# Kernel tuning notes

Hardware: AMD Instinct MI355X
Metric: run time of the kernel (lower is better)

The kernel has to match this reference:

```python
import jax, jax.numpy as jnp
import numpy as np

B, N, C = 256, 256, 128   # batch (=N_res rows), seq len, pair channels
H, D = 4, 128             # heads, per-head dim (== output_dim per module code)
O = 128                   # output_dim


def _glorot(key, shape, fan_in, fan_out):
    limit = np.sqrt(6.0 / (fan_in + fan_out))
    return jax.random.uniform(key, shape, jnp.float32, -limit, limit)


def setup_inputs() -> dict:
    key = jax.random.key(0)
    ks = jax.random.split(key, 9)
    q_data = jax.random.normal(ks[0], (B, N, C), jnp.float32)
    m_data = jax.random.normal(ks[1], (B, N, C), jnp.float32)
    bias = jax.random.normal(ks[2], (B, 1, N, N), jnp.float32)
    nonbatched_bias = jax.random.normal(ks[3], (H, N, N), jnp.float32)
    query_w = _glorot(ks[4], (C, H, D), C, H * D)
    key_w = _glorot(ks[5], (C, H, D), C, H * D)
    value_w = _glorot(ks[6], (C, H, D), C, H * D)
    gating_w = jnp.zeros((C, H, D), jnp.float32)
    gating_b = jnp.ones((H, D), jnp.float32)
    output_w = _glorot(ks[7], (H, D, O), H * D, O)
    output_b = jnp.zeros((O,), jnp.float32)
    return {
        'q_data': q_data, 'm_data': m_data, 'bias': bias,
        'nonbatched_bias': nonbatched_bias,
        'query_w': query_w, 'key_w': key_w, 'value_w': value_w,
        'gating_w': gating_w, 'gating_b': gating_b,
        'output_w': output_w, 'output_b': output_b,
    }


def reference(q_data, m_data, bias, nonbatched_bias,
              query_w, key_w, value_w, gating_w, gating_b,
              output_w, output_b):
    key_dim = query_w.shape[-1]  # per-head dim (tied to output_dim in module)
    q = jnp.einsum('bqa,ahc->bqhc', q_data, query_w) * key_dim ** (-0.5)
    k = jnp.einsum('bka,ahc->bkhc', m_data, key_w)
    v = jnp.einsum('bka,ahc->bkhc', m_data, value_w)
    logits = jnp.einsum('bqhc,bkhc->bhqk', q, k) + bias
    logits = logits + nonbatched_bias[None]  # broadcast shared bias over batch
    weights = jax.nn.softmax(logits, axis=-1)
    weighted_avg = jnp.einsum('bhqk,bkhc->bqhc', weights, v)
    gate = jax.nn.sigmoid(jnp.einsum('bqc,chv->bqhv', q_data, gating_w) + gating_b)
    weighted_avg = weighted_avg * gate
    return jnp.einsum('bqhc,hco->bqo', weighted_avg, output_w) + output_b
```

## Files before the change

kernel.cpp:

```cpp
#include <hip/hip_runtime.h>
#include <stdint.h>


typedef unsigned short u16;
typedef u16 u16x8 __attribute__((ext_vector_type(8)));
typedef u16 u16x4 __attribute__((ext_vector_type(4)));
typedef __bf16 bf16x8 __attribute__((ext_vector_type(8)));
typedef float floatx4 __attribute__((ext_vector_type(4)));

union B8 { u16x8 u; bf16x8 b; };

__device__ __forceinline__ float bf2f(u16 u) {
  union { uint32_t i; float f; } v; v.i = ((uint32_t)u) << 16; return v.f;
}
__device__ __forceinline__ u16 f2bf(float f) {
  union { float f; uint32_t i; } v; v.f = f;
  return (u16)((v.i + 0x7fffu + ((v.i >> 16) & 1u)) >> 16);
}
__device__ __forceinline__ bf16x8 ld8(const u16* p) { return *(const bf16x8*)p; }
__device__ __forceinline__ floatx4 mfma16(bf16x8 a, bf16x8 b, floatx4 c) {
  return __builtin_amdgcn_mfma_f32_16x16x32_bf16(a, b, c, 0, 0, 0);
}
__device__ __forceinline__ void cfence() { asm volatile("" ::: "memory"); }

template<bool BF>
__device__ __forceinline__ bf16x8 ldin8(const void* p, long long idx) {
  if constexpr (BF) {
    return *(const bf16x8*)((const u16*)p + idx);
  } else {
    const float* f = (const float*)p + idx;
    floatx4 a = *(const floatx4*)f;
    floatx4 b = *(const floatx4*)(f + 4);
    B8 r;
    #pragma unroll
    for (int i = 0; i < 4; ++i) { r.u[i] = f2bf(a[i]); r.u[i + 4] = f2bf(b[i]); }
    return r.b;
  }
}
template<bool BF>
__device__ __forceinline__ float ldin1(const void* p, long long idx) {
  if constexpr (BF) return bf2f(((const u16*)p)[idx]);
  else              return ((const float*)p)[idx];
}
template<bool BF>
__device__ __forceinline__ floatx4 ldin4(const void* p, long long idx) {
  floatx4 v;
  if constexpr (BF) {
    u16x4 u = *(const u16x4*)((const u16*)p + idx);
    #pragma unroll
    for (int i = 0; i < 4; ++i) v[i] = bf2f(u[i]);
  } else {
    v = *(const floatx4*)((const float*)p + idx);
  }
  return v;
}

template<bool BF>
__device__ __forceinline__ void pre_body(
    const void* qw, const void* kw, const void* vw, const void* gw,
    const void* ow, u16* wt)
{
  const int blk = blockIdx.x, tid = threadIdx.x;
  if (blk < 16) {
    const int mat = blk >> 2, h = blk & 3;
    const void* W = (mat == 0) ? qw : (mat == 1) ? kw : (mat == 2) ? vw : gw;
    u16* dst = wt + blk * 16384;
    for (int idx = tid; idx < 16384; idx += 256) {
      int c = idx >> 7, d = idx & 127;
      dst[d * 128 + c] = f2bf(ldin1<BF>(W, (long long)c * 512 + h * 128 + d));
    }
  } else {
    const int part = blk - 16;
    u16* dst = wt + 16 * 16384;
    for (int idx = tid; idx < 16384; idx += 256) {
      int k = idx >> 7, o = idx & 127;
      int kg = part * 128 + k;
      dst[o * 512 + kg] = f2bf(ldin1<BF>(ow, (long long)kg * 128 + o));
    }
  }
}

__global__ __launch_bounds__(256) void k_pre(
    const void* qw, const void* kw, const void* vw, const void* gw,
    const void* ow, const void* gating_b, u16* wt)
{
  const bool bf = (*(const uint32_t*)gating_b) == 0x3F803F80u;
  if (bf) pre_body<true >(qw, kw, vw, gw, ow, wt);
  else    pre_body<false>(qw, kw, vw, gw, ow, wt);
}

template<bool BF>
__device__ __forceinline__ void fused_body(
    const void* q_data, const void* m_data,
    const void* __restrict__ bias, const void* __restrict__ nbias,
    const void* gating_b, const u16* __restrict__ wt,
    u16* Ob, int b0, int Bc, u16* smem)
{
  const int tid  = threadIdx.x;
  const int lane = tid & 63, w = tid >> 6;
  const int quad = lane >> 4, l15 = lane & 15;
  const int l7   = l15 & 7;

  const int nwg = Bc * 4, id = blockIdx.x;
  const int xcd = id & 7, rest = id >> 3;
  const int qq = nwg >> 3, rm = nwg & 7;
  const int swz = (xcd < rm ? xcd * (qq + 1) : rm * (qq + 1) + (xcd - rm) * qq) + rest;
  const int bl = swz >> 2, h = swz & 3;
  const int bg = b0 + bl;
  const long long bh = (long long)(bl * 4 + h);

  u16* Kl  = smem;
  u16* Vtl = smem + 32768;

  const u16* wtQ = wt + (0 * 4 + h) * 16384;
  const u16* wtK = wt + (1 * 4 + h) * 16384;
  const u16* wtV = wt + (2 * 4 + h) * 16384;
  const u16* wtG = wt + (3 * 4 + h) * 16384;
  const float scale = 0.088388347648318447f;

  const int m0 = w * 16;

  bf16x8 aq[4];
  {
    u16* Qs = (w < 8) ? (Kl + w * 2176) : (Vtl + (w - 8) * 2176);
    floatx4 qa[8];
    #pragma unroll
    for (int ni = 0; ni < 8; ++ni) qa[ni] = (floatx4){0.f, 0.f, 0.f, 0.f};
    #pragma unroll
    for (int ks = 0; ks < 4; ++ks) {
      bf16x8 aA = ldin8<BF>(q_data, ((long long)bg * 256 + m0 + l15) * 128 + ks * 32 + quad * 8);
      #pragma unroll
      for (int ni = 0; ni < 8; ++ni) {
        bf16x8 bw = ld8(wtQ + (ni * 16 + l15) * 128 + ks * 32 + quad * 8);
        qa[ni] = mfma16(aA, bw, qa[ni]);
      }
    }
    #pragma unroll
    for (int ni = 0; ni < 8; ++ni)
      #pragma unroll
      for (int r = 0; r < 4; ++r)
        Qs[(quad * 4 + r) * 136 + ni * 16 + l15] = f2bf(qa[ni][r] * scale);
    cfence();
    #pragma unroll
    for (int ks = 0; ks < 4; ++ks)
      aq[ks] = ld8(Qs + l15 * 136 + ks * 32 + quad * 8);
  }
  __syncthreads();

  {
    bf16x8 aA[4];
    #pragma unroll
    for (int ks = 0; ks < 4; ++ks)
      aA[ks] = ldin8<BF>(m_data, ((long long)bg * 256 + m0 + l15) * 128 + ks * 32 + quad * 8);

    floatx4 ka[8];
    #pragma unroll
    for (int ni = 0; ni < 8; ++ni) ka[ni] = (floatx4){0.f, 0.f, 0.f, 0.f};
    #pragma unroll
    for (int ks = 0; ks < 4; ++ks)
      #pragma unroll
      for (int ni = 0; ni < 8; ++ni) {
        bf16x8 bw = ld8(wtK + (ni * 16 + l15) * 128 + ks * 32 + quad * 8);
        ka[ni] = mfma16(aA[ks], bw, ka[ni]);
      }
    #pragma unroll
    for (int ni = 0; ni < 8; ++ni)
      #pragma unroll
      for (int r = 0; r < 4; ++r) {
        int n = m0 + quad * 4 + r, d = ni * 16 + l15;
        Kl[n * 128 + (d ^ ((n & 7) << 3))] = f2bf(ka[ni][r]);
      }

    floatx4 va[8];
    #pragma unroll
    for (int ni = 0; ni < 8; ++ni) va[ni] = (floatx4){0.f, 0.f, 0.f, 0.f};
    #pragma unroll
    for (int ks = 0; ks < 4; ++ks)
      #pragma unroll
      for (int ni = 0; ni < 8; ++ni) {
        bf16x8 bw = ld8(wtV + (ni * 16 + l15) * 128 + ks * 32 + quad * 8);
        va[ni] = mfma16(aA[ks], bw, va[ni]);
      }
    #pragma unroll
    for (int ni = 0; ni < 8; ++ni) {
      int d = ni * 16 + l15, n4 = m0 + quad * 4;
      u16x4 vv;
      #pragma unroll
      for (int r = 0; r < 4; ++r) vv[r] = f2bf(va[ni][r]);
      *(u16x4*)(Vtl + d * 256 + (n4 ^ ((d & 7) << 3))) = vv;
    }
  }
  __syncthreads();

  floatx4 s[16];
  #pragma unroll
  for (int nt = 0; nt < 16; ++nt) {
    long long gi = ((long long)bg * 256 + m0 + l15) * 256 + nt * 16 + quad * 4;
    long long gn = ((long long)h  * 256 + m0 + l15) * 256 + nt * 16 + quad * 4;
    floatx4 bv = ldin4<BF>(bias, gi);
    floatx4 nv = ldin4<BF>(nbias, gn);
    #pragma unroll
    for (int r = 0; r < 4; ++r) s[nt][r] = bv[r] + nv[r];
  }
  #pragma unroll
  for (int nt = 0; nt < 16; ++nt) {
    #pragma unroll
    for (int ks = 0; ks < 4; ++ks) {
      bf16x8 kf = ld8(Kl + (nt * 16 + l15) * 128 + ((ks * 32 + quad * 8) ^ (l7 << 3)));
      s[nt] = mfma16(kf, aq[ks], s[nt]);
    }
  }

  floatx4 m4 = s[0];
  #pragma unroll
  for (int nt = 1; nt < 16; ++nt)
    #pragma unroll
    for (int r = 0; r < 4; ++r) m4[r] = fmaxf(m4[r], s[nt][r]);
  float mx = fmaxf(fmaxf(m4[0], m4[1]), fmaxf(m4[2], m4[3]));
  mx = fmaxf(mx, __shfl_xor(mx, 16));
  mx = fmaxf(mx, __shfl_xor(mx, 32));

  u16x4 pk[16];
  floatx4 s4 = (floatx4){0.f, 0.f, 0.f, 0.f};
  #pragma unroll
  for (int nt = 0; nt < 16; ++nt) {
    #pragma unroll
    for (int r = 0; r < 4; ++r) {
      float e = __expf(s[nt][r] - mx);
      s4[r] += e;
      pk[nt][r] = f2bf(e);
    }
  }
  float sm = s4[0] + s4[1] + s4[2] + s4[3];
  sm += __shfl_xor(sm, 16);
  sm += __shfl_xor(sm, 32);
  const float inv = 1.f / sm;

  __syncthreads();

  u16* Ps = Kl + w * 2048;
  floatx4 o[8];
  #pragma unroll
  for (int dt = 0; dt < 8; ++dt) o[dt] = (floatx4){0.f, 0.f, 0.f, 0.f};
  #pragma unroll
  for (int kh = 0; kh < 2; ++kh) {
    #pragma unroll
    for (int nt2 = 0; nt2 < 8; ++nt2)
      *(u16x4*)(Ps + l15 * 128 + ((nt2 * 16 + quad * 4) ^ (l7 << 3))) = pk[kh * 8 + nt2];
    cfence();
    bf16x8 ap[4];
    #pragma unroll
    for (int ks = 0; ks < 4; ++ks)
      ap[ks] = ld8(Ps + l15 * 128 + ((ks * 32 + quad * 8) ^ (l7 << 3)));
    #pragma unroll
    for (int dt = 0; dt < 8; ++dt)
      #pragma unroll
      for (int ks = 0; ks < 4; ++ks) {
        bf16x8 bv = ld8(Vtl + (dt * 16 + l15) * 256 +
                        ((kh * 128 + ks * 32 + quad * 8) ^ (l7 << 3)));
        o[dt] = mfma16(ap[ks], bv, o[dt]);
      }
    cfence();
  }

  float invq[4];
  #pragma unroll
  for (int r = 0; r < 4; ++r) invq[r] = __shfl(inv, quad * 4 + r);
  bf16x8 aqd[4];
  #pragma unroll
  for (int ks = 0; ks < 4; ++ks)
    aqd[ks] = ldin8<BF>(q_data, ((long long)bg * 256 + m0 + l15) * 128 + ks * 32 + quad * 8);
  #pragma unroll
  for (int nt = 0; nt < 8; ++nt) {
    floatx4 g = (floatx4){0.f, 0.f, 0.f, 0.f};
    #pragma unroll
    for (int ks = 0; ks < 4; ++ks) {
      bf16x8 bw = ld8(wtG + (nt * 16 + l15) * 128 + ks * 32 + quad * 8);
      g = mfma16(aqd[ks], bw, g);
    }
    #pragma unroll
    for (int r = 0; r < 4; ++r) {
      int row = m0 + quad * 4 + r, d = nt * 16 + l15;
      float gate = 1.f / (1.f + __expf(-(g[r] + ldin1<BF>(gating_b, h * 128 + d))));
      Ob[(bh * 256 + row) * 128 + d] = f2bf(o[nt][r] * invq[r] * gate);
    }
  }
}

__global__ __launch_bounds__(1024) void k_fused(
    const void* q_data, const void* m_data, const void* bias,
    const void* nbias, const void* gating_b, const u16* wt,
    u16* Ob, int b0, int Bc)
{
  __shared__ __align__(16) u16 smem[65536];
  const bool bf = (*(const uint32_t*)gating_b) == 0x3F803F80u;
  if (bf) fused_body<true >(q_data, m_data, bias, nbias, gating_b, wt, Ob, b0, Bc, smem);
  else    fused_body<false>(q_data, m_data, bias, nbias, gating_b, wt, Ob, b0, Bc, smem);
}

template<bool BF>
__device__ __forceinline__ void out_body(
    const u16* wsr, const u16* wtO, const void* output_b,
    void* out, int b0)
{
  const int tid  = threadIdx.x;
  const int lane = tid & 63, w = tid >> 6;
  const int quad = lane >> 4, l15 = lane & 15;
  const int wm = w >> 1, wn = w & 1;
  const int r0l = blockIdx.x * 32;
  const int bl  = r0l >> 8, n0 = r0l & 255;

  floatx4 acc[4];
  #pragma unroll
  for (int ni = 0; ni < 4; ++ni) acc[ni] = (floatx4){0.f, 0.f, 0.f, 0.f};

  #pragma unroll
  for (int kt = 0; kt < 4; ++kt) {
    #pragma unroll
    for (int ks = 0; ks < 4; ++ks) {
      bf16x8 af = ld8(wsr + ((long long)(bl * 4 + kt) * 256 + n0 + wm * 16 + l15) * 128
                          + ks * 32 + quad * 8);
      #pragma unroll
      for (int ni = 0; ni < 4; ++ni) {
        int col = wn * 64 + ni * 16 + l15;
        bf16x8 bw = ld8(wtO + (long long)col * 512 + kt * 128 + ks * 32 + quad * 8);
        acc[ni] = mfma16(af, bw, acc[ni]);
      }
    }
  }

  #pragma unroll
  for (int ni = 0; ni < 4; ++ni) {
    #pragma unroll
    for (int r = 0; r < 4; ++r) {
      int i = wm * 16 + quad * 4 + r;
      int j = wn * 64 + ni * 16 + l15;
      long long orow = (long long)b0 * 256 + r0l + i;
      float v = acc[ni][r] + ldin1<BF>(output_b, j);
      if constexpr (BF) ((u16*)out)[orow * 128 + j] = f2bf(v);
      else              ((float*)out)[orow * 128 + j] = v;
    }
  }
}

__global__ __launch_bounds__(256) void k_out(
    const u16* wsr, const u16* wtO, const void* output_b,
    const void* gating_b, void* out, int b0)
{
  const bool bf = (*(const uint32_t*)gating_b) == 0x3F803F80u;
  if (bf) out_body<true >(wsr, wtO, output_b, out, b0);
  else    out_body<false>(wsr, wtO, output_b, out, b0);
}

extern "C" void kernel_launch(void* const* d_in, const int* in_sizes, int n_in,
                              void* d_out, int out_size, void* d_ws, size_t ws_size,
                              hipStream_t stream)
{
  (void)in_sizes; (void)n_in; (void)out_size;
  const void* q_data   = d_in[0];
  const void* m_data   = d_in[1];
  const void* bias     = d_in[2];
  const void* nbias    = d_in[3];
  const void* query_w  = d_in[4];
  const void* key_w    = d_in[5];
  const void* value_w  = d_in[6];
  const void* gating_w = d_in[7];
  const void* gating_b = d_in[8];
  const void* output_w = d_in[9];
  const void* output_b = d_in[10];
  u16* ws = (u16*)d_ws;

  const long long wtElems = 16 * 16384 + 128 * 512;
  u16* wt  = ws;
  u16* wtO = wt + 16 * 16384;
  u16* reg = ws + wtElems;

  const size_t per_batch_bytes = 131072ull * 2;
  const size_t fixed_bytes = (size_t)wtElems * 2;
  int Bc = 1;
  while (Bc * 2 <= 256 &&
         fixed_bytes + (size_t)(Bc * 2) * per_batch_bytes <= ws_size) Bc *= 2;

  k_pre<<<20, 256, 0, stream>>>(query_w, key_w, value_w, gating_w,
                                output_w, gating_b, wt);

  for (int b0 = 0; b0 < 256; b0 += Bc) {
    k_fused<<<Bc * 4, 1024, 0, stream>>>(q_data, m_data, bias, nbias,
                                         gating_b, wt, reg, b0, Bc);
    k_out<<<8 * Bc, 256, 0, stream>>>(reg, wtO, output_b,
                                      gating_b, d_out, b0);
  }
}
```

Measured before the change: 625.1 us.

## Split attention into query halves with online softmax over key tiles

```diff
diff --git a/kernel.cpp b/kernel.cpp
--- a/kernel.cpp
+++ b/kernel.cpp
@@ -101,16 +101,15 @@
   const int quad = lane >> 4, l15 = lane & 15;
   const int l7   = l15 & 7;
 
-  const int nwg = Bc * 4, id = blockIdx.x;
-  const int xcd = id & 7, rest = id >> 3;
-  const int qq = nwg >> 3, rm = nwg & 7;
-  const int swz = (xcd < rm ? xcd * (qq + 1) : rm * (qq + 1) + (xcd - rm) * qq) + rest;
-  const int bl = swz >> 2, h = swz & 3;
+  const int nwg = Bc * 8;
+  const int id  = blockIdx.x;
+  const int swz = (id & 7) * (nwg >> 3) + (id >> 3);
+  const int bl = swz >> 3, h = (swz >> 1) & 3, qt = swz & 1;
   const int bg = b0 + bl;
   const long long bh = (long long)(bl * 4 + h);
 
-  u16* Kl  = smem;
-  u16* Vtl = smem + 32768;
+  u16* Kt = smem;
+  u16* Vt = smem + 16384;
 
   const u16* wtQ = wt + (0 * 4 + h) * 16384;
   const u16* wtK = wt + (1 * 4 + h) * 16384;
@@ -118,11 +117,11 @@
   const u16* wtG = wt + (3 * 4 + h) * 16384;
   const float scale = 0.088388347648318447f;
 
-  const int m0 = w * 16;
+  const int m0 = qt * 128 + w * 16;
 
   bf16x8 aq[4];
   {
-    u16* Qs = (w < 8) ? (Kl + w * 2176) : (Vtl + (w - 8) * 2176);
+    u16* Qs = smem + w * 2176;
     floatx4 qa[8];
     #pragma unroll
     for (int ni = 0; ni < 8; ++ni) qa[ni] = (floatx4){0.f, 0.f, 0.f, 0.f};
@@ -147,125 +146,145 @@
   }
   __syncthreads();
 
-  {
-    bf16x8 aA[4];
-    #pragma unroll
-    for (int ks = 0; ks < 4; ++ks)
-      aA[ks] = ldin8<BF>(m_data, ((long long)bg * 256 + m0 + l15) * 128 + ks * 32 + quad * 8);
-
-    floatx4 ka[8];
-    #pragma unroll
-    for (int ni = 0; ni < 8; ++ni) ka[ni] = (floatx4){0.f, 0.f, 0.f, 0.f};
-    #pragma unroll
-    for (int ks = 0; ks < 4; ++ks)
+  float m_run = -1e30f, l_run = 0.f;
+  floatx4 o[8];
+  #pragma unroll
+  for (int dt = 0; dt < 8; ++dt) o[dt] = (floatx4){0.f, 0.f, 0.f, 0.f};
+
+  #pragma unroll
+  for (int t = 0; t < 2; ++t) {
+    const int nb = t * 128 + w * 16;
+
+    {
+      bf16x8 aA[4];
+      #pragma unroll
+      for (int ks = 0; ks < 4; ++ks)
+        aA[ks] = ldin8<BF>(m_data, ((long long)bg * 256 + nb + l15) * 128 + ks * 32 + quad * 8);
+
+      floatx4 ka[8];
+      #pragma unroll
+      for (int ni = 0; ni < 8; ++ni) ka[ni] = (floatx4){0.f, 0.f, 0.f, 0.f};
+      #pragma unroll
+      for (int ks = 0; ks < 4; ++ks)
+        #pragma unroll
+        for (int ni = 0; ni < 8; ++ni) {
+          bf16x8 bw = ld8(wtK + (ni * 16 + l15) * 128 + ks * 32 + quad * 8);
+          ka[ni] = mfma16(aA[ks], bw, ka[ni]);
+        }
+      #pragma unroll
+      for (int ni = 0; ni < 8; ++ni)
+        #pragma unroll
+        for (int r = 0; r < 4; ++r) {
+          int nl = w * 16 + quad * 4 + r, d = ni * 16 + l15;
+          Kt[nl * 128 + (d ^ ((nl & 7) << 3))] = f2bf(ka[ni][r]);
+        }
+
+      floatx4 va[8];
+      #pragma unroll
+      for (int ni = 0; ni < 8; ++ni) va[ni] = (floatx4){0.f, 0.f, 0.f, 0.f};
+      #pragma unroll
+      for (int ks = 0; ks < 4; ++ks)
+        #pragma unroll
+        for (int ni = 0; ni < 8; ++ni) {
+          bf16x8 bw = ld8(wtV + (ni * 16 + l15) * 128 + ks * 32 + quad * 8);
+          va[ni] = mfma16(aA[ks], bw, va[ni]);
+        }
       #pragma unroll
       for (int ni = 0; ni < 8; ++ni) {
-        bf16x8 bw = ld8(wtK + (ni * 16 + l15) * 128 + ks * 32 + quad * 8);
-        ka[ni] = mfma16(aA[ks], bw, ka[ni]);
-      }
-    #pragma unroll
-    for (int ni = 0; ni < 8; ++ni)
+        int d = ni * 16 + l15, n4 = w * 16 + quad * 4;
+        u16x4 vv;
+        #pragma unroll
+        for (int r = 0; r < 4; ++r) vv[r] = f2bf(va[ni][r]);
+        *(u16x4*)(Vt + d * 128 + (n4 ^ ((d & 7) << 3))) = vv;
+      }
+    }
+
+    floatx4 bz[8];
+    #pragma unroll
+    for (int j = 0; j < 8; ++j) {
+      long long gi = ((long long)bg * 256 + m0 + l15) * 256 + t * 128 + j * 16 + quad * 4;
+      long long gn = ((long long)h  * 256 + m0 + l15) * 256 + t * 128 + j * 16 + quad * 4;
+      floatx4 bv = ldin4<BF>(bias, gi);
+      floatx4 nv = ldin4<BF>(nbias, gn);
+      #pragma unroll
+      for (int r = 0; r < 4; ++r) bz[j][r] = bv[r] + nv[r];
+    }
+    __syncthreads();
+
+    floatx4 s[8];
+    #pragma unroll
+    for (int j = 0; j < 8; ++j) s[j] = bz[j];
+    __builtin_amdgcn_s_setprio(1);
+    #pragma unroll
+    for (int j = 0; j < 8; ++j)
+      #pragma unroll
+      for (int ks = 0; ks < 4; ++ks) {
+        bf16x8 kf = ld8(Kt + (j * 16 + l15) * 128 + ((ks * 32 + quad * 8) ^ (l7 << 3)));
+        s[j] = mfma16(kf, aq[ks], s[j]);
+      }
+    __builtin_amdgcn_s_setprio(0);
+
+    float mxt = -1e30f;
+    #pragma unroll
+    for (int j = 0; j < 8; ++j)
+      #pragma unroll
+      for (int r = 0; r < 4; ++r) mxt = fmaxf(mxt, s[j][r]);
+    mxt = fmaxf(mxt, __shfl_xor(mxt, 16));
+    mxt = fmaxf(mxt, __shfl_xor(mxt, 32));
+    const float mnew = fmaxf(m_run, mxt);
+    const float a = __expf(m_run - mnew);
+    m_run = mnew;
+
+    float lsum = 0.f;
+    u16x4 pk[8];
+    #pragma unroll
+    for (int j = 0; j < 8; ++j)
       #pragma unroll
       for (int r = 0; r < 4; ++r) {
-        int n = m0 + quad * 4 + r, d = ni * 16 + l15;
-        Kl[n * 128 + (d ^ ((n & 7) << 3))] = f2bf(ka[ni][r]);
-      }
-
-    floatx4 va[8];
-    #pragma unroll
-    for (int ni = 0; ni < 8; ++ni) va[ni] = (floatx4){0.f, 0.f, 0.f, 0.f};
-    #pragma unroll
-    for (int ks = 0; ks < 4; ++ks)
-      #pragma unroll
-      for (int ni = 0; ni < 8; ++ni) {
-        bf16x8 bw = ld8(wtV + (ni * 16 + l15) * 128 + ks * 32 + quad * 8);
-        va[ni] = mfma16(aA[ks], bw, va[ni]);
-      }
-    #pragma unroll
-    for (int ni = 0; ni < 8; ++ni) {
-      int d = ni * 16 + l15, n4 = m0 + quad * 4;
-      u16x4 vv;
-      #pragma unroll
-      for (int r = 0; r < 4; ++r) vv[r] = f2bf(va[ni][r]);
-      *(u16x4*)(Vtl + d * 256 + (n4 ^ ((d & 7) << 3))) = vv;
-    }
-  }
-  __syncthreads();
-
-  floatx4 s[16];
-  #pragma unroll
-  for (int nt = 0; nt < 16; ++nt) {
-    long long gi = ((long long)bg * 256 + m0 + l15) * 256 + nt * 16 + quad * 4;
-    long long gn = ((long long)h  * 256 + m0 + l15) * 256 + nt * 16 + quad * 4;
-    floatx4 bv = ldin4<BF>(bias, gi);
-    floatx4 nv = ldin4<BF>(nbias, gn);
-    #pragma unroll
-    for (int r = 0; r < 4; ++r) s[nt][r] = bv[r] + nv[r];
-  }
-  #pragma unroll
-  for (int nt = 0; nt < 16; ++nt) {
-    #pragma unroll
-    for (int ks = 0; ks < 4; ++ks) {
-      bf16x8 kf = ld8(Kl + (nt * 16 + l15) * 128 + ((ks * 32 + quad * 8) ^ (l7 << 3)));
-      s[nt] = mfma16(kf, aq[ks], s[nt]);
-    }
-  }
-
-  floatx4 m4 = s[0];
-  #pragma unroll
-  for (int nt = 1; nt < 16; ++nt)
-    #pragma unroll
-    for (int r = 0; r < 4; ++r) m4[r] = fmaxf(m4[r], s[nt][r]);
-  float mx = fmaxf(fmaxf(m4[0], m4[1]), fmaxf(m4[2], m4[3]));
-  mx = fmaxf(mx, __shfl_xor(mx, 16));
-  mx = fmaxf(mx, __shfl_xor(mx, 32));
-
-  u16x4 pk[16];
-  floatx4 s4 = (floatx4){0.f, 0.f, 0.f, 0.f};
-  #pragma unroll
-  for (int nt = 0; nt < 16; ++nt) {
-    #pragma unroll
-    for (int r = 0; r < 4; ++r) {
-      float e = __expf(s[nt][r] - mx);
-      s4[r] += e;
-      pk[nt][r] = f2bf(e);
-    }
-  }
-  float sm = s4[0] + s4[1] + s4[2] + s4[3];
-  sm += __shfl_xor(sm, 16);
-  sm += __shfl_xor(sm, 32);
-  const float inv = 1.f / sm;
-
-  __syncthreads();
-
-  u16* Ps = Kl + w * 2048;
-  floatx4 o[8];
-  #pragma unroll
-  for (int dt = 0; dt < 8; ++dt) o[dt] = (floatx4){0.f, 0.f, 0.f, 0.f};
-  #pragma unroll
-  for (int kh = 0; kh < 2; ++kh) {
-    #pragma unroll
-    for (int nt2 = 0; nt2 < 8; ++nt2)
-      *(u16x4*)(Ps + l15 * 128 + ((nt2 * 16 + quad * 4) ^ (l7 << 3))) = pk[kh * 8 + nt2];
+        float e = __expf(s[j][r] - mnew);
+        lsum += e;
+        pk[j][r] = f2bf(e);
+      }
+    lsum += __shfl_xor(lsum, 16);
+    lsum += __shfl_xor(lsum, 32);
+    l_run = l_run * a + lsum;
+
+    float a4[4];
+    #pragma unroll
+    for (int r = 0; r < 4; ++r) a4[r] = __shfl(a, quad * 4 + r);
+    #pragma unroll
+    for (int dt = 0; dt < 8; ++dt)
+      #pragma unroll
+      for (int r = 0; r < 4; ++r) o[dt][r] *= a4[r];
+
+    __syncthreads();
+
+    u16* Ps = Kt + w * 2048;
+    #pragma unroll
+    for (int j = 0; j < 8; ++j)
+      *(u16x4*)(Ps + l15 * 128 + ((j * 16 + quad * 4) ^ (l7 << 3))) = pk[j];
     cfence();
     bf16x8 ap[4];
     #pragma unroll
     for (int ks = 0; ks < 4; ++ks)
       ap[ks] = ld8(Ps + l15 * 128 + ((ks * 32 + quad * 8) ^ (l7 << 3)));
+    __builtin_amdgcn_s_setprio(1);
     #pragma unroll
     for (int dt = 0; dt < 8; ++dt)
       #pragma unroll
       for (int ks = 0; ks < 4; ++ks) {
-        bf16x8 bv = ld8(Vtl + (dt * 16 + l15) * 256 +
-                        ((kh * 128 + ks * 32 + quad * 8) ^ (l7 << 3)));
+        bf16x8 bv = ld8(Vt + (dt * 16 + l15) * 128 + ((ks * 32 + quad * 8) ^ (l7 << 3)));
         o[dt] = mfma16(ap[ks], bv, o[dt]);
       }
-    cfence();
-  }
-
+    __builtin_amdgcn_s_setprio(0);
+    __syncthreads();
+  }
+
+  const float inv = 1.f / l_run;
   float invq[4];
   #pragma unroll
   for (int r = 0; r < 4; ++r) invq[r] = __shfl(inv, quad * 4 + r);
+
   bf16x8 aqd[4];
   #pragma unroll
   for (int ks = 0; ks < 4; ++ks)
@@ -287,12 +306,12 @@
   }
 }
 
-__global__ __launch_bounds__(1024) void k_fused(
+__global__ __launch_bounds__(512, 4) void k_fused(
     const void* q_data, const void* m_data, const void* bias,
     const void* nbias, const void* gating_b, const u16* wt,
     u16* Ob, int b0, int Bc)
 {
-  __shared__ __align__(16) u16 smem[65536];
+  __shared__ __align__(16) u16 smem[32768];
   const bool bf = (*(const uint32_t*)gating_b) == 0x3F803F80u;
   if (bf) fused_body<true >(q_data, m_data, bias, nbias, gating_b, wt, Ob, b0, Bc, smem);
   else    fused_body<false>(q_data, m_data, bias, nbias, gating_b, wt, Ob, b0, Bc, smem);
@@ -307,7 +326,7 @@
   const int lane = tid & 63, w = tid >> 6;
   const int quad = lane >> 4, l15 = lane & 15;
   const int wm = w >> 1, wn = w & 1;
-  const int r0l = blockIdx.x * 32;
+  const int r0l = blockIdx.x * 64;
   const int bl  = r0l >> 8, n0 = r0l & 255;
 
   floatx4 acc[4];
@@ -316,17 +335,19 @@
 
   #pragma unroll
   for (int kt = 0; kt < 4; ++kt) {
-    #pragma unroll
-    for (int ks = 0; ks < 4; ++ks) {
-      bf16x8 af = ld8(wsr + ((long long)(bl * 4 + kt) * 256 + n0 + wm * 16 + l15) * 128
-                          + ks * 32 + quad * 8);
+    bf16x8 af[4];
+    #pragma unroll
+    for (int ks = 0; ks < 4; ++ks)
+      af[ks] = ld8(wsr + ((long long)(bl * 4 + kt) * 256 + n0 + wm * 16 + l15) * 128
+                       + ks * 32 + quad * 8);
+    #pragma unroll
+    for (int ks = 0; ks < 4; ++ks)
       #pragma unroll
       for (int ni = 0; ni < 4; ++ni) {
         int col = wn * 64 + ni * 16 + l15;
         bf16x8 bw = ld8(wtO + (long long)col * 512 + kt * 128 + ks * 32 + quad * 8);
-        acc[ni] = mfma16(af, bw, acc[ni]);
-      }
-    }
+        acc[ni] = mfma16(af[ks], bw, acc[ni]);
+      }
   }
 
   #pragma unroll
@@ -343,7 +364,7 @@
   }
 }
 
-__global__ __launch_bounds__(256) void k_out(
+__global__ __launch_bounds__(512, 2) void k_out(
     const u16* wsr, const u16* wtO, const void* output_b,
     const void* gating_b, void* out, int b0)
 {
@@ -385,9 +406,9 @@
                                 output_w, gating_b, wt);
 
   for (int b0 = 0; b0 < 256; b0 += Bc) {
-    k_fused<<<Bc * 4, 1024, 0, stream>>>(q_data, m_data, bias, nbias,
-                                         gating_b, wt, reg, b0, Bc);
-    k_out<<<8 * Bc, 256, 0, stream>>>(reg, wtO, output_b,
+    k_fused<<<Bc * 8, 512, 0, stream>>>(q_data, m_data, bias, nbias,
+                                        gating_b, wt, reg, b0, Bc);
+    k_out<<<Bc * 4, 512, 0, stream>>>(reg, wtO, output_b,
                                       gating_b, d_out, b0);
   }
 }
```

Result: slower. 1.011 ms (+61.7%).
